# Kernel tuning notes

Measured on AMD Instinct MI355X. Metric: run time of the kernel, lower is better.

The kernel has to match this reference:

```python
import jax, jax.numpy as jnp
import numpy as np

SPP_SIZES = (1, 3, 6, 8)  # -> 1+9+36+64 = 110 pooled tokens


def conv1x1(x, w, b):
    # x: [B,C,H,W], w: [O,C], b: [O] -> [B,O,H,W]
    return jnp.einsum('bchw,oc->bohw', x, w) + b[None, :, None, None]


def spp(t):
    # t: [B,C,H,W] with H,W divisible by every size -> [B,C,110]
    B, C, H, W = t.shape
    outs = []
    for s in SPP_SIZES:
        p = t.reshape(B, C, s, H // s, s, W // s).mean(axis=(3, 5))
        outs.append(p.reshape(B, C, s * s))
    return jnp.concatenate(outs, axis=-1)


def setup_inputs() -> dict:
    key = jax.random.key(0)
    ks = jax.random.split(key, 9)
    B, C, H, W = 8, 512, 96, 96
    inner = 256
    sc = 1.0 / np.sqrt(C)
    return {
        'x': jax.random.normal(ks[0], (B, C, H, W), dtype=jnp.float32),
        'phi_w': jax.random.normal(ks[1], (inner, C), dtype=jnp.float32) * sc,
        'phi_b': jnp.zeros((inner,), dtype=jnp.float32),
        'theta_w': jax.random.normal(ks[2], (inner, C), dtype=jnp.float32) * sc,
        'theta_b': jnp.zeros((inner,), dtype=jnp.float32),
        'gamma_w': jax.random.normal(ks[3], (inner, C), dtype=jnp.float32) * sc,
        'gamma_b': jnp.zeros((inner,), dtype=jnp.float32),
        'W_w': jax.random.normal(ks[4], (C, inner), dtype=jnp.float32) * (1.0 / np.sqrt(inner)),
        'W_b': jnp.zeros((C,), dtype=jnp.float32),
    }


def reference(x, phi_w, phi_b, theta_w, theta_b, gamma_w, gamma_b, W_w, W_b):
    B, C, H, W = x.shape
    HW = H * W
    phi = jax.nn.relu(conv1x1(x, phi_w, phi_b))      # [B,256,H,W]
    theta = jax.nn.relu(conv1x1(x, theta_w, theta_b))
    gamma = conv1x1(x, gamma_w, gamma_b)
    theta_p = spp(theta)                              # [B,256,110]
    gamma_p = spp(gamma)                              # [B,256,110]
    # Faithful to original: raw reshape (NOT a transpose) of [B,256,H,W] -> [B,HW,256]
    phi_r = jnp.reshape(phi, (B, HW, 256))
    y1 = jnp.einsum('bnc,bck->bnk', phi_r, theta_p)   # [B,HW,110]
    y1_norm = jax.nn.softmax(y1 * (HW ** -0.25), axis=-1)
    y2 = jnp.einsum('bnk,bkc->bnc', y1_norm, jnp.transpose(gamma_p, (0, 2, 1)))  # [B,HW,256]
    # Faithful raw reshape back to [B,256,H,W]
    y2_r = jnp.reshape(y2, (B, 256, H, W))
    y2_w = conv1x1(y2_r, W_w, W_b)                    # [B,C,H,W]
    return x + y2_w
```

## Files before the change

kernel.cpp:

```cpp
#include <hip/hip_runtime.h>

#define NB 8
#define CIN 512
#define OIN 256
#define HWN 9216
#define KP 110
#define SCL 0.10206207261596577f

typedef __attribute__((ext_vector_type(8))) short bf16x8;
typedef __attribute__((ext_vector_type(4))) float f32x4;
typedef unsigned short u16;

__device__ inline unsigned bf16_1(float a) {
    unsigned u = __builtin_bit_cast(unsigned, a);
    return (u + 0x7fffu + ((u >> 16) & 1u)) >> 16;
}
__device__ inline unsigned bf16_pack(float a, float b) {
    return bf16_1(a) | (bf16_1(b) << 16);
}
__device__ inline float b2f(u16 u) {
    return __builtin_bit_cast(float, ((unsigned)u) << 16);
}

__device__ __forceinline__ void gload16(const u16* g, u16* l) {
    __builtin_amdgcn_global_load_lds(
        (const __attribute__((address_space(1))) unsigned int*)g,
        (__attribute__((address_space(3))) unsigned int*)l, 16, 0, 0);
}

__global__ __launch_bounds__(256) void castw_kernel(
    const float* __restrict__ phi_w, const float* __restrict__ theta_w,
    const float* __restrict__ Ww,
    u16* __restrict__ Wcat, u16* __restrict__ Wwb)
{
    int i = blockIdx.x * 256 + threadIdx.x;
    if (i < 262144) {
        float v = (i < 131072) ? phi_w[i] : theta_w[i - 131072];
        Wcat[i] = (u16)bf16_1(v);
    } else {
        int j = i - 262144;
        Wwb[j] = (u16)bf16_1(Ww[j]);
    }
}

__global__ __launch_bounds__(256) void castx_kernel(
    const float* __restrict__ x, u16* __restrict__ xT)
{
    const int t = threadIdx.x;
    const int tx = t & 15, ty = t >> 4;
    const int b = blockIdx.z;
    const int c0 = blockIdx.y * 64;
    const int hw0 = blockIdx.x * 64;

    const float* xb = x + ((size_t)b * CIN + c0 + ty * 4) * HWN + hw0 + tx * 4;
    float4 v[4];
#pragma unroll
    for (int q = 0; q < 4; ++q)
        v[q] = *(const float4*)(xb + (size_t)q * HWN);

    u16* dst = xT + ((size_t)b * HWN + hw0 + tx * 4) * CIN + c0 + ty * 4;
    const float* f = (const float*)v;
#pragma unroll
    for (int p = 0; p < 4; ++p) {
        uint2 o = {bf16_pack(f[0 * 4 + p], f[1 * 4 + p]),
                   bf16_pack(f[2 * 4 + p], f[3 * 4 + p])};
        *(uint2*)(dst + (size_t)p * CIN) = o;
    }
}

template<int KDIM, int MODE>
__global__ __launch_bounds__(256, 3) void gemm_kernel(
    const u16* __restrict__ A,
    const u16* __restrict__ Bw,
    const float* __restrict__ b0, const float* __restrict__ b1,
    const float* __restrict__ resid,
    void* __restrict__ out0_, void* __restrict__ out1_)
{
    __shared__ u16 As[3][128 * 32];
    __shared__ u16 Bs[3][128 * 32];

    constexpr int NSTEP = KDIM / 32;
    constexpr int NWG = 72 * 4 * NB;

    const int id = blockIdx.x;
    const int swz = (id & 7) * (NWG / 8) + (id >> 3);
    const int u = swz % 288;
    const int bz = swz / 288;
    const int by = u & 3;
    const int bx = u >> 2;

    const int t = threadIdx.x;
    const int m0 = bx * 128;
    const int n0 = by * 128;
    const int w = t >> 6, l = t & 63;
    const int wr = w >> 1, wc = w & 1;
    const int g = l >> 4, li = l & 15;

    const u16* Ab = A + (size_t)bz * HWN * KDIM + (size_t)m0 * KDIM;
    const u16* Bb = Bw + (size_t)n0 * KDIM;

    f32x4 zero = {0.f, 0.f, 0.f, 0.f};
    f32x4 acc[4][4];
#pragma unroll
    for (int i = 0; i < 4; ++i)
#pragma unroll
        for (int j = 0; j < 4; ++j) acc[i][j] = zero;

    auto stage = [&](int step) {
        const int buf = step % 3;
#pragma unroll
        for (int j = 0; j < 2; ++j) {
            int c = j * 256 + t;
            int row = c >> 2, slot = c & 3;
            int ss = slot ^ ((row >> 1) & 3);
            gload16(Ab + (size_t)row * KDIM + step * 32 + ss * 8, &As[buf][c * 8]);
        }
#pragma unroll
        for (int j = 0; j < 2; ++j) {
            int c = j * 256 + t;
            int row = c >> 2, slot = c & 3;
            int ss = slot ^ ((row >> 1) & 3);
            gload16(Bb + (size_t)row * KDIM + step * 32 + ss * 8, &Bs[buf][c * 8]);
        }
    };

    stage(0);
    stage(1);

#pragma unroll 1
    for (int s = 0; s < NSTEP; ++s) {
        if (s + 2 < NSTEP) {
            stage(s + 2);
            asm volatile("s_waitcnt vmcnt(8)" ::: "memory");
        } else if (s + 1 < NSTEP) {
            asm volatile("s_waitcnt vmcnt(4)" ::: "memory");
        } else {
            asm volatile("s_waitcnt vmcnt(0)" ::: "memory");
        }
        __builtin_amdgcn_s_barrier();
        __builtin_amdgcn_sched_barrier(0);

        const int cb = s % 3;
        bf16x8 af[4], bv[4];
#pragma unroll
        for (int mi = 0; mi < 4; ++mi) {
            int r = wr * 64 + mi * 16 + li;
            int sl = g ^ ((r >> 1) & 3);
            af[mi] = *(const bf16x8*)&As[cb][r * 32 + sl * 8];
        }
#pragma unroll
        for (int ni = 0; ni < 4; ++ni) {
            int r = wc * 64 + ni * 16 + li;
            int sl = g ^ ((r >> 1) & 3);
            bv[ni] = *(const bf16x8*)&Bs[cb][r * 32 + sl * 8];
        }
#pragma unroll
        for (int mi = 0; mi < 4; ++mi)
#pragma unroll
            for (int ni = 0; ni < 4; ++ni)
                acc[mi][ni] = __builtin_amdgcn_mfma_f32_16x16x32_bf16(
                    af[mi], bv[ni], acc[mi][ni], 0, 0, 0);

        __builtin_amdgcn_s_barrier();
    }

#pragma unroll
    for (int ni = 0; ni < 4; ++ni) {
        int n = n0 + wc * 64 + ni * 16 + li;
        if constexpr (MODE == 0) {
            float bias = (n < 256) ? b0[n] : b1[n - 256];
            u16* dst = (u16*)((n < 256) ? out0_ : out1_) + ((size_t)bz * 256 + (n & 255)) * HWN;
#pragma unroll
            for (int mi = 0; mi < 4; ++mi) {
                int m = m0 + wr * 64 + mi * 16 + (g << 2);
                f32x4 v = acc[mi][ni];
                float e0 = fmaxf(v.x + bias, 0.f), e1 = fmaxf(v.y + bias, 0.f);
                float e2 = fmaxf(v.z + bias, 0.f), e3 = fmaxf(v.w + bias, 0.f);
                uint2 pk = {bf16_pack(e0, e1), bf16_pack(e2, e3)};
                *(uint2*)(dst + m) = pk;
            }
        } else {
            float bias = b0[n];
            float* dst = (float*)out0_ + ((size_t)bz * 512 + n) * HWN;
            const float* res = resid + ((size_t)bz * 512 + n) * HWN;
#pragma unroll
            for (int mi = 0; mi < 4; ++mi) {
                int m = m0 + wr * 64 + mi * 16 + (g << 2);
                f32x4 v = acc[mi][ni];
                float4 rx = *(const float4*)(res + m);
                float4 o = {v.x + bias + rx.x, v.y + bias + rx.y,
                            v.z + bias + rx.z, v.w + bias + rx.w};
                *(float4*)(dst + m) = o;
            }
        }
    }
}

__global__ __launch_bounds__(256) void pool_x_kernel(
    const float* __restrict__ in, float* __restrict__ out)
{
    __shared__ float ps[576];
    const int plane = blockIdx.x;
    const float* p = in + (size_t)plane * HWN;
    const int t = threadIdx.x;

    for (int i = t; i < 576; i += 256) {
        int bh = i / 24, bw = i % 24;
        float s = 0.f;
#pragma unroll
        for (int r = 0; r < 4; ++r) {
            float4 v = *(const float4*)&p[(bh * 4 + r) * 96 + bw * 4];
            s += v.x + v.y + v.z + v.w;
        }
        ps[i] = s;
    }
    __syncthreads();

    if (t < KP) {
        float s = 0.f;
        if (t == 0) {
            for (int i = 0; i < 576; ++i) s += ps[i];
            s *= (1.0f / 9216.0f);
        } else if (t < 10) {
            int idx = t - 1, bi = idx / 3, bj = idx % 3;
            for (int r = 0; r < 8; ++r)
                for (int c = 0; c < 8; ++c)
                    s += ps[(bi * 8 + r) * 24 + bj * 8 + c];
            s *= (1.0f / 1024.0f);
        } else if (t < 46) {
            int idx = t - 10, bi = idx / 6, bj = idx % 6;
            for (int r = 0; r < 4; ++r)
                for (int c = 0; c < 4; ++c)
                    s += ps[(bi * 4 + r) * 24 + bj * 4 + c];
            s *= (1.0f / 256.0f);
        } else {
            int idx = t - 46, bi = idx / 8, bj = idx % 8;
            for (int r = 0; r < 3; ++r)
                for (int c = 0; c < 3; ++c)
                    s += ps[(bi * 3 + r) * 24 + bj * 3 + c];
            s *= (1.0f / 144.0f);
        }
        out[(size_t)plane * KP + t] = s;
    }
}

__global__ __launch_bounds__(256) void pool_t_kernel(
    const u16* __restrict__ in, u16* __restrict__ outT)
{
    __shared__ float ps[576];
    const int plane = blockIdx.x;
    const int b = plane >> 8, c = plane & 255;
    const u16* p = in + (size_t)plane * HWN;
    const int t = threadIdx.x;

    for (int i = t; i < 576; i += 256) {
        int bh = i / 24, bw = i % 24;
        float s = 0.f;
#pragma unroll
        for (int r = 0; r < 4; ++r) {
            ushort4 v = *(const ushort4*)&p[(bh * 4 + r) * 96 + bw * 4];
            s += b2f(v.x) + b2f(v.y) + b2f(v.z) + b2f(v.w);
        }
        ps[i] = s;
    }
    __syncthreads();

    if (t < 128) {
        float s = 0.f;
        if (t == 0) {
            for (int i = 0; i < 576; ++i) s += ps[i];
            s *= (1.0f / 9216.0f);
        } else if (t < 10) {
            int idx = t - 1, bi = idx / 3, bj = idx % 3;
            for (int r = 0; r < 8; ++r)
                for (int cc = 0; cc < 8; ++cc)
                    s += ps[(bi * 8 + r) * 24 + bj * 8 + cc];
            s *= (1.0f / 1024.0f);
        } else if (t < 46) {
            int idx = t - 10, bi = idx / 6, bj = idx % 6;
            for (int r = 0; r < 4; ++r)
                for (int cc = 0; cc < 4; ++cc)
                    s += ps[(bi * 4 + r) * 24 + bj * 4 + cc];
            s *= (1.0f / 256.0f);
        } else if (t < KP) {
            int idx = t - 46, bi = idx / 8, bj = idx % 8;
            for (int r = 0; r < 3; ++r)
                for (int cc = 0; cc < 3; ++cc)
                    s += ps[(bi * 3 + r) * 24 + bj * 3 + cc];
            s *= (1.0f / 144.0f);
        } else {
            s = 0.f;
        }
        outT[((size_t)b * 128 + t) * 256 + c] = (u16)bf16_1(s);
    }
}

__global__ __launch_bounds__(256) void gammap_kernel(
    const float* __restrict__ xp,
    const float* __restrict__ gw,
    const float* __restrict__ gb,
    u16* __restrict__ gp)
{
    __shared__ float xc[8][512];
    const int kb = blockIdx.x * 8, b = blockIdx.y;
    const int t = threadIdx.x;

#pragma unroll
    for (int j = 0; j < 16; ++j) {
        int idx = j * 256 + t;
        int kk = idx >> 9, c = idx & 511;
        int k = kb + kk;
        xc[kk][c] = (k < KP) ? xp[((size_t)b * CIN + c) * KP + k] : 0.f;
    }
    __syncthreads();

    float bias = gb[t];
    float acc[8];
#pragma unroll
    for (int kk = 0; kk < 8; ++kk) acc[kk] = bias;

    const float* wrow = gw + (size_t)t * CIN;
#pragma unroll 2
    for (int c = 0; c < CIN; c += 4) {
        float4 wv = *(const float4*)&wrow[c];
#pragma unroll
        for (int kk = 0; kk < 8; ++kk) {
            acc[kk] = fmaf(wv.x, xc[kk][c], acc[kk]);
            acc[kk] = fmaf(wv.y, xc[kk][c + 1], acc[kk]);
            acc[kk] = fmaf(wv.z, xc[kk][c + 2], acc[kk]);
            acc[kk] = fmaf(wv.w, xc[kk][c + 3], acc[kk]);
        }
    }

    ushort4 o0, o1;
    o0.x = (u16)bf16_1(acc[0]); o0.y = (u16)bf16_1(acc[1]);
    o0.z = (u16)bf16_1(acc[2]); o0.w = (u16)bf16_1(acc[3]);
    o1.x = (u16)bf16_1(acc[4]); o1.y = (u16)bf16_1(acc[5]);
    o1.z = (u16)bf16_1(acc[6]); o1.w = (u16)bf16_1(acc[7]);
    u16* dst = gp + ((size_t)b * 256 + t) * 128 + kb;
    *(ushort4*)(dst) = o0;
    *(ushort4*)(dst + 4) = o1;
}

__global__ __launch_bounds__(256, 4) void attn_kernel(
    const u16* __restrict__ phi,
    const u16* __restrict__ tpT,
    const u16* __restrict__ gp,
    u16* __restrict__ y2T)
{
    __shared__ __align__(16) char smem[40960];
    u16* As = (u16*)smem;
    u16* Bs = (u16*)(smem + 8192);
    char* Pb = smem + 24576;
    u16* Gs = (u16*)smem;

    const int t = threadIdx.x;
    const int w = t >> 6, l = t & 63;
    const int g = l >> 4, li = l & 15;
    const int b = blockIdx.y;
    const int rr = blockIdx.x >> 2;
    const int ci0 = (blockIdx.x & 3) << 6;

    const u16* phib = phi + (size_t)b * (OIN * HWN);
    const u16* tpb  = tpT + (size_t)b * (128 * 256);
    const u16* gpb  = gp  + (size_t)b * (256 * 128);

    const int srow = t >> 3;
    const int su = t & 7;

    f32x4 zero = {0.f, 0.f, 0.f, 0.f};
    f32x4 acc[8];
#pragma unroll
    for (int j = 0; j < 8; ++j) acc[j] = zero;

    for (int kt = 0; kt < 256; kt += 64) {
#pragma unroll
        for (int cc = 0; cc < 2; ++cc) {
            int row = cc * 32 + srow;
            int ss = su ^ (row & 7);
            gload16(phib + (size_t)(ci0 + row) * HWN + rr * 256 + kt + ss * 8,
                    &As[(row * 8 + su) * 8]);
        }
#pragma unroll
        for (int cc = 0; cc < 4; ++cc) {
            int row = cc * 32 + srow;
            int ss = su ^ (row & 7);
            gload16(tpb + (size_t)row * 256 + kt + ss * 8,
                    &Bs[(row * 8 + su) * 8]);
        }
        __syncthreads();

#pragma unroll
        for (int h = 0; h < 2; ++h) {
            int r = w * 16 + li;
            bf16x8 af = *(const bf16x8*)&As[r * 64 + (((h * 4 + g) ^ (r & 7)) << 3)];
            bf16x8 bfr[8];
#pragma unroll
            for (int ni = 0; ni < 8; ++ni) {
                int rb = ni * 16 + li;
                bfr[ni] = *(const bf16x8*)&Bs[rb * 64 + (((h * 4 + g) ^ (rb & 7)) << 3)];
            }
#pragma unroll
            for (int ni = 0; ni < 8; ++ni)
                acc[ni] = __builtin_amdgcn_mfma_f32_16x16x32_bf16(
                    af, bfr[ni], acc[ni], 0, 0, 0);
        }
        __syncthreads();
    }

    bool vm[8];
#pragma unroll
    for (int ni = 0; ni < 8; ++ni) vm[ni] = (ni * 16 + li) < KP;

#pragma unroll
    for (int r = 0; r < 4; ++r) {
        float mx = -1e30f;
#pragma unroll
        for (int ni = 0; ni < 8; ++ni)
            if (vm[ni]) mx = fmaxf(mx, acc[ni][r] * SCL);
        mx = fmaxf(mx, __shfl_xor(mx, 1));
        mx = fmaxf(mx, __shfl_xor(mx, 2));
        mx = fmaxf(mx, __shfl_xor(mx, 4));
        mx = fmaxf(mx, __shfl_xor(mx, 8));
        float s = 0.f;
#pragma unroll
        for (int ni = 0; ni < 8; ++ni) {
            float e = vm[ni] ? __expf(acc[ni][r] * SCL - mx) : 0.f;
            acc[ni][r] = e;
            s += e;
        }
        s += __shfl_xor(s, 1);
        s += __shfl_xor(s, 2);
        s += __shfl_xor(s, 4);
        s += __shfl_xor(s, 8);
        float inv = 1.0f / s;
#pragma unroll
        for (int ni = 0; ni < 8; ++ni) acc[ni][r] *= inv;
    }
#pragma unroll
    for (int ni = 0; ni < 8; ++ni)
#pragma unroll
        for (int r = 0; r < 4; ++r) {
            int row = w * 16 + g * 4 + r;
            int col = ni * 16 + li;
            *(short*)(Pb + row * 256 + (((col >> 3) ^ (row & 7)) << 4) + ((col & 7) << 1)) =
                (short)bf16_1(acc[ni][r]);
        }

    f32x4 acc2[16];
#pragma unroll
    for (int j = 0; j < 16; ++j) acc2[j] = zero;

#pragma unroll 1
    for (int ch = 0; ch < 4; ++ch) {
#pragma unroll
        for (int j = 0; j < 4; ++j) {
            int row = j * 64 + (t >> 2);
            int slot = t & 3;
            int ss = slot ^ (row & 3);
            gload16(gpb + (size_t)row * 128 + ch * 32 + ss * 8,
                    &Gs[(j * 256 + t) * 8]);
        }
        __syncthreads();

        int prow = w * 16 + li;
        bf16x8 a2 = *(const bf16x8*)(Pb + prow * 256 + (((ch * 4 + g) ^ (prow & 7)) << 4));
#pragma unroll
        for (int cf = 0; cf < 16; ++cf) {
            int crow = cf * 16 + li;
            bf16x8 bv = *(const bf16x8*)((const char*)Gs + crow * 64 + ((g ^ (crow & 3)) << 4));
            acc2[cf] = __builtin_amdgcn_mfma_f32_16x16x32_bf16(a2, bv, acc2[cf], 0, 0, 0);
        }
        __syncthreads();
    }

#pragma unroll
    for (int cf = 0; cf < 16; ++cf) {
        int c = cf * 16 + li;
        int cib = w * 16 + g * 4;
        int e0 = c * 64 + (cib ^ ((li & 7) << 3));
        unsigned d0 = bf16_pack(acc2[cf][0], acc2[cf][1]);
        unsigned d1 = bf16_pack(acc2[cf][2], acc2[cf][3]);
        *(unsigned*)(smem + (size_t)e0 * 2) = d0;
        *(unsigned*)(smem + (size_t)e0 * 2 + 4) = d1;
    }

    __syncthreads();

    {
        int c = t;
        u16* dst = y2T + ((size_t)b * HWN + rr * 256 + c) * 256 + ci0;
#pragma unroll
        for (int j = 0; j < 8; ++j) {
            uint4 v = *(const uint4*)(smem + c * 128 + ((j ^ (c & 7)) << 4));
            *(uint4*)(dst + j * 8) = v;
        }
    }
}

extern "C" void kernel_launch(void* const* d_in, const int* in_sizes, int n_in,
                              void* d_out, int out_size, void* d_ws, size_t ws_size,
                              hipStream_t stream)
{
    const float* x       = (const float*)d_in[0];
    const float* phi_w   = (const float*)d_in[1];
    const float* phi_b   = (const float*)d_in[2];
    const float* theta_w = (const float*)d_in[3];
    const float* theta_b = (const float*)d_in[4];
    const float* gamma_w = (const float*)d_in[5];
    const float* gamma_b = (const float*)d_in[6];
    const float* W_w     = (const float*)d_in[7];
    const float* W_b     = (const float*)d_in[8];
    float* out = (float*)d_out;

    char* p = (char*)d_ws;
    u16* xT     = (u16*)p;  p += (size_t)NB * HWN * CIN * 2;
    u16* phi_bf = (u16*)p;  p += (size_t)NB * OIN * HWN * 2;
    u16* th_y2  = (u16*)p;  p += (size_t)NB * OIN * HWN * 2;
    float* xp   = (float*)p; p += (size_t)NB * CIN * KP * 4;
    u16* tpT    = (u16*)p;  p += (size_t)NB * 128 * 256 * 2;
    u16* gp     = (u16*)p;  p += (size_t)NB * 256 * 128 * 2;
    u16* Wcat   = (u16*)p;  p += 512 * 512 * 2;
    u16* Wwb    = (u16*)p;  p += 512 * 256 * 2;

    castw_kernel<<<1536, 256, 0, stream>>>(phi_w, theta_w, W_w, Wcat, Wwb);
    castx_kernel<<<dim3(144, 8, NB), 256, 0, stream>>>(x, xT);
    pool_x_kernel<<<dim3(NB * CIN), 256, 0, stream>>>(x, xp);
    gemm_kernel<512, 0><<<dim3(72 * 4 * NB), 256, 0, stream>>>(
        xT, Wcat, phi_b, theta_b, nullptr, phi_bf, th_y2);
    pool_t_kernel<<<dim3(NB * OIN), 256, 0, stream>>>(th_y2, tpT);
    gammap_kernel<<<dim3(16, NB), 256, 0, stream>>>(xp, gamma_w, gamma_b, gp);
    attn_kernel<<<dim3(144, NB), 256, 0, stream>>>(phi_bf, tpT, gp, th_y2);
    gemm_kernel<256, 1><<<dim3(72 * 4 * NB), 256, 0, stream>>>(
        th_y2, Wwb, W_b, nullptr, x, out, nullptr);
}
```

Measured before the change: 306.4 us.

## Add 512-thread 256x128-tile bf16 GEMM with split-K triple-buffered pipeline

```diff
diff --git a/kernel.cpp b/kernel.cpp
--- a/kernel.cpp
+++ b/kernel.cpp
@@ -27,6 +27,8 @@
         (const __attribute__((address_space(1))) unsigned int*)g,
         (__attribute__((address_space(3))) unsigned int*)l, 16, 0, 0);
 }
+
+#define CFENCE asm volatile("" ::: "memory")
 
 __global__ __launch_bounds__(256) void castw_kernel(
     const float* __restrict__ phi_w, const float* __restrict__ theta_w,
@@ -66,6 +68,134 @@
                    bf16_pack(f[2 * 4 + p], f[3 * 4 + p])};
         *(uint2*)(dst + (size_t)p * CIN) = o;
     }
+}
+
+template<int KDIM, int MODE>
+__global__ __launch_bounds__(512, 2) void gemm8p_kernel(
+    const u16* __restrict__ A,
+    const u16* __restrict__ Bw,
+    const float* __restrict__ b0, const float* __restrict__ b1,
+    void* __restrict__ out0_, void* __restrict__ out1_)
+{
+    extern __shared__ u16 smemd[];
+    constexpr int NT = KDIM / 64;
+    constexpr int NWG = 36 * 4 * NB;
+
+    const int id = blockIdx.x;
+    const int swz = (id & 7) * (NWG / 8) + (id >> 3);
+    const int u = swz % 144;
+    const int bz = swz / 144;
+    const int by = u & 3;
+    const int bx = u >> 2;
+
+    const int tid = threadIdx.x;
+    const int wid = tid >> 6, l = tid & 63;
+    const int wm = wid >> 1, wn = wid & 1;
+    const int g = l >> 4, li = l & 15;
+
+    const int m0 = bx * 256, n0 = by * 128;
+    const u16* Ab = A + (size_t)bz * HWN * KDIM + (size_t)m0 * KDIM;
+    const u16* Bb = Bw + (size_t)n0 * KDIM;
+
+    f32x4 zero = {0.f, 0.f, 0.f, 0.f};
+    f32x4 acc[4][4];
+#pragma unroll
+    for (int i = 0; i < 4; ++i)
+#pragma unroll
+        for (int j = 0; j < 4; ++j) acc[i][j] = zero;
+
+    auto stage = [&](int tile, int kh) {
+        const int buf = tile % 3;
+        const int aoff = (buf * 2 + kh) * 8192;
+#pragma unroll
+        for (int j = 0; j < 2; ++j) {
+            int c = j * 512 + tid;
+            int row = c >> 2, sl = c & 3;
+            int ss = sl ^ (row & 3);
+            gload16(Ab + (size_t)row * KDIM + tile * 64 + kh * 32 + ss * 8,
+                    &smemd[aoff + c * 8]);
+        }
+        const int boff = 49152 + (buf * 2 + kh) * 4096;
+        {
+            int c = tid;
+            int row = c >> 2, sl = c & 3;
+            int ss = sl ^ (row & 3);
+            gload16(Bb + (size_t)row * KDIM + tile * 64 + kh * 32 + ss * 8,
+                    &smemd[boff + c * 8]);
+        }
+    };
+
+    auto compute = [&](int tile, int kh) {
+        const int buf = tile % 3;
+        const u16* Ar = &smemd[(buf * 2 + kh) * 8192];
+        const u16* Br = &smemd[49152 + (buf * 2 + kh) * 4096];
+        bf16x8 af[4], bfr[4];
+#pragma unroll
+        for (int mi = 0; mi < 4; ++mi) {
+            int r = wm * 64 + mi * 16 + li;
+            af[mi] = *(const bf16x8*)&Ar[r * 32 + ((g ^ (r & 3)) << 3)];
+        }
+#pragma unroll
+        for (int ni = 0; ni < 4; ++ni) {
+            int rb = wn * 64 + ni * 16 + li;
+            bfr[ni] = *(const bf16x8*)&Br[rb * 32 + ((g ^ (rb & 3)) << 3)];
+        }
+        __builtin_amdgcn_s_setprio(1);
+#pragma unroll
+        for (int mi = 0; mi < 4; ++mi)
+#pragma unroll
+            for (int ni = 0; ni < 4; ++ni)
+                acc[mi][ni] = __builtin_amdgcn_mfma_f32_16x16x32_bf16(
+                    af[mi], bfr[ni], acc[mi][ni], 0, 0, 0);
+        __builtin_amdgcn_s_setprio(0);
+    };
+
+#define PH_BAR { CFENCE; __builtin_amdgcn_s_barrier(); CFENCE; }
+
+    stage(0, 0); stage(0, 1); stage(1, 0); stage(1, 1);
+
+#pragma unroll 1
+    for (int t = 0; t < NT - 2; ++t) {
+        stage(t + 2, 0);
+        asm volatile("s_waitcnt vmcnt(12)" ::: "memory");
+        PH_BAR;
+        compute(t, 0);
+        stage(t + 2, 1);
+        asm volatile("s_waitcnt vmcnt(12)" ::: "memory");
+        PH_BAR;
+        compute(t, 1);
+    }
+    asm volatile("s_waitcnt vmcnt(9)" ::: "memory");
+    PH_BAR;
+    compute(NT - 2, 0);
+    asm volatile("s_waitcnt vmcnt(6)" ::: "memory");
+    PH_BAR;
+    compute(NT - 2, 1);
+    asm volatile("s_waitcnt vmcnt(3)" ::: "memory");
+    PH_BAR;
+    compute(NT - 1, 0);
+    asm volatile("s_waitcnt vmcnt(0)" ::: "memory");
+    PH_BAR;
+    compute(NT - 1, 1);
+
+#pragma unroll
+    for (int ni = 0; ni < 4; ++ni) {
+        int n = n0 + wn * 64 + ni * 16 + li;
+        if constexpr (MODE == 0) {
+            float bias = (n < 256) ? b0[n] : b1[n - 256];
+            u16* dst = (u16*)((n < 256) ? out0_ : out1_) + ((size_t)bz * 256 + (n & 255)) * HWN;
+#pragma unroll
+            for (int mi = 0; mi < 4; ++mi) {
+                int m = m0 + wm * 64 + mi * 16 + (g << 2);
+                f32x4 v = acc[mi][ni];
+                float e0 = fmaxf(v.x + bias, 0.f), e1 = fmaxf(v.y + bias, 0.f);
+                float e2 = fmaxf(v.z + bias, 0.f), e3 = fmaxf(v.w + bias, 0.f);
+                uint2 pk = {bf16_pack(e0, e1), bf16_pack(e2, e3)};
+                *(uint2*)(dst + m) = pk;
+            }
+        }
+    }
+#undef PH_BAR
 }
 
 template<int KDIM, int MODE>
@@ -523,11 +653,14 @@
     u16* Wcat   = (u16*)p;  p += 512 * 512 * 2;
     u16* Wwb    = (u16*)p;  p += 512 * 256 * 2;
 
+    hipFuncSetAttribute(reinterpret_cast<const void*>(&gemm8p_kernel<512, 0>),
+                        hipFuncAttributeMaxDynamicSharedMemorySize, 147456);
+
     castw_kernel<<<1536, 256, 0, stream>>>(phi_w, theta_w, W_w, Wcat, Wwb);
     castx_kernel<<<dim3(144, 8, NB), 256, 0, stream>>>(x, xT);
     pool_x_kernel<<<dim3(NB * CIN), 256, 0, stream>>>(x, xp);
-    gemm_kernel<512, 0><<<dim3(72 * 4 * NB), 256, 0, stream>>>(
-        xT, Wcat, phi_b, theta_b, nullptr, phi_bf, th_y2);
+    gemm8p_kernel<512, 0><<<dim3(36 * 4 * NB), 512, 147456, stream>>>(
+        xT, Wcat, phi_b, theta_b, phi_bf, th_y2);
     pool_t_kernel<<<dim3(NB * OIN), 256, 0, stream>>>(th_y2, tpT);
     gammap_kernel<<<dim3(16, NB), 256, 0, stream>>>(xp, gamma_w, gamma_b, gp);
     attn_kernel<<<dim3(144, NB), 256, 0, stream>>>(phi_bf, tpT, gp, th_y2);
```

Measured after the change: 318.9 us. 4.1% more time.

## Pool x from bf16 transposed copy via two-stage block-sum kernels

Applied to the files above, without the earlier changes.

```diff
diff --git a/kernel.cpp b/kernel.cpp
--- a/kernel.cpp
+++ b/kernel.cpp
@@ -65,6 +65,91 @@
         uint2 o = {bf16_pack(f[0 * 4 + p], f[1 * 4 + p]),
                    bf16_pack(f[2 * 4 + p], f[3 * 4 + p])};
         *(uint2*)(dst + (size_t)p * CIN) = o;
+    }
+}
+
+__global__ __launch_bounds__(256) void poolx_bs_kernel(
+    const u16* __restrict__ xT,
+    float* __restrict__ bs)
+{
+    __shared__ float sm[4][512];
+    const int bh = blockIdx.x, b = blockIdx.y;
+    const int t = threadIdx.x;
+    const int g = t >> 6;
+    const int co = (t & 63) * 8;
+
+#pragma unroll 1
+    for (int bw = 0; bw < 24; ++bw) {
+        float a[8] = {0.f, 0.f, 0.f, 0.f, 0.f, 0.f, 0.f, 0.f};
+        const int hwbase = (bh * 4 + g) * 96 + bw * 4;
+        const u16* base = xT + ((size_t)b * HWN + hwbase) * CIN + co;
+#pragma unroll
+        for (int wI = 0; wI < 4; ++wI) {
+            uint4 v = *(const uint4*)(base + (size_t)wI * CIN);
+            a[0] += b2f((u16)v.x); a[1] += b2f((u16)(v.x >> 16));
+            a[2] += b2f((u16)v.y); a[3] += b2f((u16)(v.y >> 16));
+            a[4] += b2f((u16)v.z); a[5] += b2f((u16)(v.z >> 16));
+            a[6] += b2f((u16)v.w); a[7] += b2f((u16)(v.w >> 16));
+        }
+#pragma unroll
+        for (int j = 0; j < 8; ++j) sm[g][co + j] = a[j];
+        __syncthreads();
+        {
+            int c2 = t * 2;
+            float s0 = sm[0][c2] + sm[1][c2] + sm[2][c2] + sm[3][c2];
+            float s1 = sm[0][c2 + 1] + sm[1][c2 + 1] + sm[2][c2 + 1] + sm[3][c2 + 1];
+            bs[((size_t)b * CIN + c2) * 576 + bh * 24 + bw] = s0;
+            bs[((size_t)b * CIN + c2 + 1) * 576 + bh * 24 + bw] = s1;
+        }
+        __syncthreads();
+    }
+}
+
+__global__ __launch_bounds__(256, 2) void poolx_fin_kernel(
+    const float* __restrict__ bs,
+    float* __restrict__ xp)
+{
+    __shared__ float ls[32][576];
+    const int c0 = blockIdx.x * 32, b = blockIdx.y;
+    const int t = threadIdx.x;
+
+#pragma unroll 1
+    for (int r = 0; r < 32; ++r) {
+        if (t < 144)
+            *(float4*)&ls[r][t * 4] =
+                *(const float4*)&bs[((size_t)b * CIN + c0 + r) * 576 + t * 4];
+    }
+    __syncthreads();
+
+    const int cl = t >> 3, w8 = t & 7;
+    const float* row = ls[cl];
+    float* xpr = xp + ((size_t)b * CIN + c0 + cl) * KP;
+#pragma unroll 1
+    for (int k = w8; k < KP; k += 8) {
+        float s = 0.f, scl;
+        if (k == 0) {
+            for (int i = 0; i < 576; ++i) s += row[i];
+            scl = 1.0f / 9216.0f;
+        } else if (k < 10) {
+            int idx = k - 1, bi = idx / 3, bj = idx % 3;
+            for (int r = 0; r < 8; ++r)
+                for (int cc = 0; cc < 8; ++cc)
+                    s += row[(bi * 8 + r) * 24 + bj * 8 + cc];
+            scl = 1.0f / 1024.0f;
+        } else if (k < 46) {
+            int idx = k - 10, bi = idx / 6, bj = idx % 6;
+            for (int r = 0; r < 4; ++r)
+                for (int cc = 0; cc < 4; ++cc)
+                    s += row[(bi * 4 + r) * 24 + bj * 4 + cc];
+            scl = 1.0f / 256.0f;
+        } else {
+            int idx = k - 46, bi = idx / 8, bj = idx % 8;
+            for (int r = 0; r < 3; ++r)
+                for (int cc = 0; cc < 3; ++cc)
+                    s += row[(bi * 3 + r) * 24 + bj * 3 + cc];
+            scl = 1.0f / 144.0f;
+        }
+        xpr[k] = s * scl;
     }
 }
 
@@ -193,54 +278,6 @@
                 *(float4*)(dst + m) = o;
             }
         }
-    }
-}
-
-__global__ __launch_bounds__(256) void pool_x_kernel(
-    const float* __restrict__ in, float* __restrict__ out)
-{
-    __shared__ float ps[576];
-    const int plane = blockIdx.x;
-    const float* p = in + (size_t)plane * HWN;
-    const int t = threadIdx.x;
-
-    for (int i = t; i < 576; i += 256) {
-        int bh = i / 24, bw = i % 24;
-        float s = 0.f;
-#pragma unroll
-        for (int r = 0; r < 4; ++r) {
-            float4 v = *(const float4*)&p[(bh * 4 + r) * 96 + bw * 4];
-            s += v.x + v.y + v.z + v.w;
-        }
-        ps[i] = s;
-    }
-    __syncthreads();
-
-    if (t < KP) {
-        float s = 0.f;
-        if (t == 0) {
-            for (int i = 0; i < 576; ++i) s += ps[i];
-            s *= (1.0f / 9216.0f);
-        } else if (t < 10) {
-            int idx = t - 1, bi = idx / 3, bj = idx % 3;
-            for (int r = 0; r < 8; ++r)
-                for (int c = 0; c < 8; ++c)
-                    s += ps[(bi * 8 + r) * 24 + bj * 8 + c];
-            s *= (1.0f / 1024.0f);
-        } else if (t < 46) {
-            int idx = t - 10, bi = idx / 6, bj = idx % 6;
-            for (int r = 0; r < 4; ++r)
-                for (int c = 0; c < 4; ++c)
-                    s += ps[(bi * 4 + r) * 24 + bj * 4 + c];
-            s *= (1.0f / 256.0f);
-        } else {
-            int idx = t - 46, bi = idx / 8, bj = idx % 8;
-            for (int r = 0; r < 3; ++r)
-                for (int c = 0; c < 3; ++c)
-                    s += ps[(bi * 3 + r) * 24 + bj * 3 + c];
-            s *= (1.0f / 144.0f);
-        }
-        out[(size_t)plane * KP + t] = s;
     }
 }
 
@@ -522,10 +559,12 @@
     u16* gp     = (u16*)p;  p += (size_t)NB * 256 * 128 * 2;
     u16* Wcat   = (u16*)p;  p += 512 * 512 * 2;
     u16* Wwb    = (u16*)p;  p += 512 * 256 * 2;
+    float* bs   = (float*)p; p += (size_t)NB * CIN * 576 * 4;
 
     castw_kernel<<<1536, 256, 0, stream>>>(phi_w, theta_w, W_w, Wcat, Wwb);
     castx_kernel<<<dim3(144, 8, NB), 256, 0, stream>>>(x, xT);
-    pool_x_kernel<<<dim3(NB * CIN), 256, 0, stream>>>(x, xp);
+    poolx_bs_kernel<<<dim3(24, NB), 256, 0, stream>>>(xT, bs);
+    poolx_fin_kernel<<<dim3(16, NB), 256, 0, stream>>>(bs, xp);
     gemm_kernel<512, 0><<<dim3(72 * 4 * NB), 256, 0, stream>>>(
         xT, Wcat, phi_b, theta_b, nullptr, phi_bf, th_y2);
     pool_t_kernel<<<dim3(NB * OIN), 256, 0, stream>>>(th_y2, tpT);
```

Result: slower. 320.5 us (median of 2 runs) (+4.6%).
